# Optimization experiments

Measured on AMD Instinct MI355X. Metric: run time of the kernel, lower is better.

The kernel has to match this reference:

```python
import jax, jax.numpy as jnp
import numpy as np

EPS = 1e-08


def setup_inputs() -> dict:
    key = jax.random.key(0)
    k1, k2, k3 = jax.random.split(key, 3)
    B = 131072
    LIP_DIM = 20
    POSE_DIM = 6
    K = LIP_DIM + POSE_DIM  # 26
    return {
        "input": jax.random.normal(k1, (B, K), dtype=jnp.float32),
        "pose_weight": jax.random.normal(k2, (512, POSE_DIM), dtype=jnp.float32),
        "weight": jax.random.normal(k3, (512, LIP_DIM), dtype=jnp.float32),
    }


def reference(input, pose_weight, weight):
    # weight: (512, lip_dim), pose_weight: (512, pose_dim) -> (512, K)
    w = jnp.concatenate([weight, pose_weight], axis=-1) + EPS
    # reduced QR (torch.qr default): Q (512, K)
    Q, R = jnp.linalg.qr(w, mode="reduced")
    Q = Q.astype(jnp.float32)
    # Original: sum_k diag_embed(input) @ Q.T over dim=1
    #   == for each batch b: sum_k input[b,k] * Q[:,k] == input @ Q.T
    # Fused equivalent avoids the (B, K, K) / (B, K, 512) intermediates.
    out = input @ Q.T  # (B, 512)
    return out
```

## Files before the change

kernel.cpp:

```cpp
#include <hip/hip_runtime.h>
#include <hip/hip_bf16.h>

#define EPSV 1e-8f
#define WSTRIDE 516

typedef float f32x4 __attribute__((ext_vector_type(4)));

__device__ __forceinline__ float rdlane(float v, int l) {
    return __int_as_float(__builtin_amdgcn_readlane(__float_as_int(v), l));
}

__device__ __forceinline__ void load_w_row(const float* __restrict__ lip_w,
                                           const float* __restrict__ pose_w,
                                           int row, float* w) {
    const float4* lp4 = reinterpret_cast<const float4*>(lip_w + row * 20);
    float4 t0 = lp4[0], t1 = lp4[1], t2 = lp4[2], t3 = lp4[3], t4 = lp4[4];
    const float2* pp2 = reinterpret_cast<const float2*>(pose_w + row * 6);
    float2 u0 = pp2[0], u1 = pp2[1], u2 = pp2[2];
    w[0]  = t0.x + EPSV; w[1]  = t0.y + EPSV; w[2]  = t0.z + EPSV; w[3]  = t0.w + EPSV;
    w[4]  = t1.x + EPSV; w[5]  = t1.y + EPSV; w[6]  = t1.z + EPSV; w[7]  = t1.w + EPSV;
    w[8]  = t2.x + EPSV; w[9]  = t2.y + EPSV; w[10] = t2.z + EPSV; w[11] = t2.w + EPSV;
    w[12] = t3.x + EPSV; w[13] = t3.y + EPSV; w[14] = t3.z + EPSV; w[15] = t3.w + EPSV;
    w[16] = t4.x + EPSV; w[17] = t4.y + EPSV; w[18] = t4.z + EPSV; w[19] = t4.w + EPSV;
    w[20] = u0.x + EPSV; w[21] = u0.y + EPSV;
    w[22] = u1.x + EPSV; w[23] = u1.y + EPSV;
    w[24] = u2.x + EPSV; w[25] = u2.y + EPSV;
}

template<int J>
struct QRStep {
    static __device__ __forceinline__ void run(float (&P)[26], float (&R)[26],
                                               const float (&Gr)[26], const int tid) {
        float sig = rdlane(Gr[J], J);
        float dot = 0.f;
#pragma unroll
        for (int i = 0; i < 26; ++i) {
            if (i < J) {
                const float rij = rdlane(R[i], J);
                sig = fmaf(-rij, rij, sig);
                dot = fmaf(rij, R[i], dot);
            }
        }
        const float alpha  = rdlane(P[J], J);
        const float S      = Gr[J] - dot - alpha * P[J];
        const float normx  = sqrtf(sig);
        const float beta   = (alpha >= 0.f) ? -normx : normx;
        const float tau    = (beta - alpha) / beta;
        const float rdenom = 1.f / (alpha - beta);
        const float dc     = fmaf(S, rdenom, P[J]);
        R[J] = (tid == J) ? beta : fmaf(-tau, dc, P[J]);
        const float trd = tau * rdenom;
#pragma unroll
        for (int i = 0; i < 26; ++i) {
            if (i > J) {
                const float pij = rdlane(P[i], J);
                P[i] = fmaf(-(trd * pij), dc, P[i]);
            }
        }
    }
};

template<int J> struct QRSteps {
    static __device__ __forceinline__ void run(float (&P)[26], float (&R)[26],
                                               const float (&Gr)[26], int tid) {
        QRStep<J>::run(P, R, Gr, tid);
        QRSteps<J + 1>::run(P, R, Gr, tid);
    }
};
template<> struct QRSteps<26> {
    static __device__ __forceinline__ void run(float (&)[26], float (&)[26],
                                               const float (&)[26], int) {}
};

__global__ __launch_bounds__(512) void qr_kernel(const float* __restrict__ pose_w,
                                                 const float* __restrict__ lip_w,
                                                 float* __restrict__ qt) {
    __shared__ float Wc[26 * WSTRIDE];
    __shared__ float G[26 * 27 + 8];
    __shared__ float Rlds[26][27];
    __shared__ float Rinv[26][27];

    const int tid = threadIdx.x;

    {
        float w[26];
        load_w_row(lip_w, pose_w, tid, w);
#pragma unroll
        for (int c = 0; c < 26; ++c) Wc[c * WSTRIDE + tid] = w[c];
    }
    __syncthreads();

    if (tid < 45) {
        int tm = 0, rem = tid;
        while (rem >= 9 - tm) { rem -= 9 - tm; ++tm; }
        const int tn = tm + rem;
        const int ra = (tm * 3 > 23) ? 23 : tm * 3;
        const int ca = (tn * 3 > 23) ? 23 : tn * 3;
        const f32x4* A0 = reinterpret_cast<const f32x4*>(&Wc[(ra + 0) * WSTRIDE]);
        const f32x4* A1 = reinterpret_cast<const f32x4*>(&Wc[(ra + 1) * WSTRIDE]);
        const f32x4* A2 = reinterpret_cast<const f32x4*>(&Wc[(ra + 2) * WSTRIDE]);
        const f32x4* B0 = reinterpret_cast<const f32x4*>(&Wc[(ca + 0) * WSTRIDE]);
        const f32x4* B1 = reinterpret_cast<const f32x4*>(&Wc[(ca + 1) * WSTRIDE]);
        const f32x4* B2 = reinterpret_cast<const f32x4*>(&Wc[(ca + 2) * WSTRIDE]);
        float acc[3][3] = {{0.f, 0.f, 0.f}, {0.f, 0.f, 0.f}, {0.f, 0.f, 0.f}};
#pragma unroll 4
        for (int i = 0; i < 128; ++i) {
            const f32x4 av[3] = {A0[i], A1[i], A2[i]};
            const f32x4 bv[3] = {B0[i], B1[i], B2[i]};
#pragma unroll
            for (int r = 0; r < 3; ++r) {
#pragma unroll
                for (int c = 0; c < 3; ++c) {
                    acc[r][c] = fmaf(av[r].x, bv[c].x, acc[r][c]);
                    acc[r][c] = fmaf(av[r].y, bv[c].y, acc[r][c]);
                    acc[r][c] = fmaf(av[r].z, bv[c].z, acc[r][c]);
                    acc[r][c] = fmaf(av[r].w, bv[c].w, acc[r][c]);
                }
            }
        }
#pragma unroll
        for (int r = 0; r < 3; ++r) {
#pragma unroll
            for (int c = 0; c < 3; ++c) {
                G[(ra + r) * 27 + (ca + c)] = acc[r][c];
                G[(ca + c) * 27 + (ra + r)] = acc[r][c];
            }
        }
    }
    __syncthreads();

    if (tid < 64) {
        const int cc = (tid < 26) ? tid : 25;
        float P[26], R[26], Gr[26];
        {
            const f32x4* pc = reinterpret_cast<const f32x4*>(&Wc[cc * WSTRIDE]);
            const f32x4 q0 = pc[0], q1 = pc[1], q2 = pc[2], q3 = pc[3],
                        q4 = pc[4], q5 = pc[5], q6 = pc[6];
            P[0]=q0.x;  P[1]=q0.y;  P[2]=q0.z;  P[3]=q0.w;
            P[4]=q1.x;  P[5]=q1.y;  P[6]=q1.z;  P[7]=q1.w;
            P[8]=q2.x;  P[9]=q2.y;  P[10]=q2.z; P[11]=q2.w;
            P[12]=q3.x; P[13]=q3.y; P[14]=q3.z; P[15]=q3.w;
            P[16]=q4.x; P[17]=q4.y; P[18]=q4.z; P[19]=q4.w;
            P[20]=q5.x; P[21]=q5.y; P[22]=q5.z; P[23]=q5.w;
            P[24]=q6.x; P[25]=q6.y;
        }
#pragma unroll
        for (int j = 0; j < 26; ++j) Gr[j] = G[j * 27 + cc];

        QRSteps<0>::run(P, R, Gr, tid);

        if (tid < 26) {
#pragma unroll
            for (int i = 0; i < 26; ++i)
                if (i <= tid) Rlds[i][tid] = R[i];
        }

        if (tid < 26) {
            float ri[26];
#pragma unroll
            for (int k = 25; k >= 0; --k) {
                float s = (k == tid) ? 1.f : 0.f;
#pragma unroll
                for (int m = 25; m > k; --m)
                    if (m <= tid) s = fmaf(-Rlds[k][m], ri[m], s);
                ri[k] = s / Rlds[k][k];
            }
#pragma unroll
            for (int k = 0; k < 26; ++k)
                if (k <= tid) Rinv[k][tid] = ri[k];
        }
    }
    __syncthreads();

    if (tid < 128) {
        float w0[26], w1[26], w2[26], w3[26];
        load_w_row(lip_w, pose_w, tid,       w0);
        load_w_row(lip_w, pose_w, tid + 128, w1);
        load_w_row(lip_w, pose_w, tid + 256, w2);
        load_w_row(lip_w, pose_w, tid + 384, w3);
#pragma unroll
        for (int k = 0; k < 26; ++k) {
            float q0 = 0.f, q1 = 0.f, q2 = 0.f, q3 = 0.f;
#pragma unroll
            for (int m = 0; m < 26; ++m) {
                if (m <= k) {
                    const float r = Rinv[m][k];
                    q0 = fmaf(w0[m], r, q0);
                    q1 = fmaf(w1[m], r, q1);
                    q2 = fmaf(w2[m], r, q2);
                    q3 = fmaf(w3[m], r, q3);
                }
            }
            float* qk = qt + k * 512 + tid;
            qk[0]   = q0;
            qk[128] = q1;
            qk[256] = q2;
            qk[384] = q3;
        }
    }
}


__global__ __launch_bounds__(256) void out_gemm(const float* __restrict__ in,
                                                const float* __restrict__ qt,
                                                float* __restrict__ out) {
    __shared__ float xs[832];
    const int tid = threadIdx.x;
    const long base = (long)blockIdx.x * 32;

    const float4* ip4 = reinterpret_cast<const float4*>(in + base * 26);
    if (tid < 208) reinterpret_cast<float4*>(xs)[tid] = ip4[tid];

    const int cg = tid & 127;
    const int rh = tid >> 7;

    float4 qf[26];
#pragma unroll
    for (int k = 0; k < 26; ++k)
        qf[k] = *reinterpret_cast<const float4*>(qt + k * 512 + cg * 4);
    __syncthreads();

    float* op = out + (base + (long)rh * 16) * 512 + cg * 4;
#pragma unroll
    for (int r = 0; r < 16; ++r) {
        const float* xr = xs + (rh * 16 + r) * 26;
        float ax = 0.f, ay = 0.f, az = 0.f, aw = 0.f;
#pragma unroll
        for (int k = 0; k < 26; ++k) {
            const float x = xr[k];
            ax = fmaf(x, qf[k].x, ax);
            ay = fmaf(x, qf[k].y, ay);
            az = fmaf(x, qf[k].z, az);
            aw = fmaf(x, qf[k].w, aw);
        }
        f32x4 o;
        o.x = ax; o.y = ay; o.z = az; o.w = aw;
        __builtin_nontemporal_store(o, reinterpret_cast<f32x4*>(op + (long)r * 512));
    }
}


extern "C" void kernel_launch(void* const* d_in, const int* in_sizes, int n_in,
                              void* d_out, int out_size, void* d_ws, size_t ws_size,
                              hipStream_t stream) {
    const float* input  = (const float*)d_in[0];
    const float* pose_w = (const float*)d_in[1];
    const float* lip_w  = (const float*)d_in[2];
    float* out = (float*)d_out;
    float* qt  = (float*)d_ws;

    const int B = in_sizes[0] / 26;

    qr_kernel<<<1, 512, 0, stream>>>(pose_w, lip_w, qt);
    out_gemm<<<(B + 31) / 32, 256, 0, stream>>>(input, qt, out);
}
```

Before: 82.45 us.

## Split Gram reduction across all waves and vectorize LDS reads in output GEMM

```diff
diff --git a/kernel.cpp b/kernel.cpp
--- a/kernel.cpp
+++ b/kernel.cpp
@@ -76,11 +76,14 @@
                                                  const float* __restrict__ lip_w,
                                                  float* __restrict__ qt) {
     __shared__ float Wc[26 * WSTRIDE];
+    __shared__ float Gp[8][26][27];
     __shared__ float G[26 * 27 + 8];
     __shared__ float Rlds[26][27];
     __shared__ float Rinv[26][27];
 
-    const int tid = threadIdx.x;
+    const int tid  = threadIdx.x;
+    const int lane = tid & 63;
+    const int wid  = tid >> 6;
 
     {
         float w[26];
@@ -90,8 +93,8 @@
     }
     __syncthreads();
 
-    if (tid < 45) {
-        int tm = 0, rem = tid;
+    if (lane < 45) {
+        int tm = 0, rem = lane;
         while (rem >= 9 - tm) { rem -= 9 - tm; ++tm; }
         const int tn = tm + rem;
         const int ra = (tm * 3 > 23) ? 23 : tm * 3;
@@ -103,8 +106,10 @@
         const f32x4* B1 = reinterpret_cast<const f32x4*>(&Wc[(ca + 1) * WSTRIDE]);
         const f32x4* B2 = reinterpret_cast<const f32x4*>(&Wc[(ca + 2) * WSTRIDE]);
         float acc[3][3] = {{0.f, 0.f, 0.f}, {0.f, 0.f, 0.f}, {0.f, 0.f, 0.f}};
+        const int i0 = 16 * wid;
 #pragma unroll 4
-        for (int i = 0; i < 128; ++i) {
+        for (int ii = 0; ii < 16; ++ii) {
+            const int i = i0 + ii;
             const f32x4 av[3] = {A0[i], A1[i], A2[i]};
             const f32x4 bv[3] = {B0[i], B1[i], B2[i]};
 #pragma unroll
@@ -122,10 +127,22 @@
         for (int r = 0; r < 3; ++r) {
 #pragma unroll
             for (int c = 0; c < 3; ++c) {
-                G[(ra + r) * 27 + (ca + c)] = acc[r][c];
-                G[(ca + c) * 27 + (ra + r)] = acc[r][c];
-            }
-        }
+                Gp[wid][ra + r][ca + c] = acc[r][c];
+                Gp[wid][ca + c][ra + r] = acc[r][c];
+            }
+        }
+    }
+    __syncthreads();
+
+    if (tid < 351) {
+        int r = 0, t = tid;
+        while (t >= 26 - r) { t -= 26 - r; ++r; }
+        const int c = r + t;
+        float s = 0.f;
+#pragma unroll
+        for (int w8 = 0; w8 < 8; ++w8) s += Gp[w8][r][c];
+        G[r * 27 + c] = s;
+        G[c * 27 + r] = s;
     }
     __syncthreads();
 
@@ -204,38 +221,61 @@
 __global__ __launch_bounds__(256) void out_gemm(const float* __restrict__ in,
                                                 const float* __restrict__ qt,
                                                 float* __restrict__ out) {
-    __shared__ float xs[832];
+    __shared__ __align__(16) float xs[32 * 28];
     const int tid = threadIdx.x;
     const long base = (long)blockIdx.x * 32;
 
-    const float4* ip4 = reinterpret_cast<const float4*>(in + base * 26);
-    if (tid < 208) reinterpret_cast<float4*>(xs)[tid] = ip4[tid];
+    if (tid < 208) {
+        const float4 v = reinterpret_cast<const float4*>(in + base * 26)[tid];
+        const float vals[4] = {v.x, v.y, v.z, v.w};
+        const int e0 = tid * 4;
+#pragma unroll
+        for (int q = 0; q < 4; ++q) {
+            const int e = e0 + q;
+            const int r = e / 26;
+            const int c = e - r * 26;
+            xs[r * 28 + c] = vals[q];
+        }
+    }
 
     const int cg = tid & 127;
     const int rh = tid >> 7;
 
-    float4 qf[26];
+    f32x4 qf[26];
 #pragma unroll
     for (int k = 0; k < 26; ++k)
-        qf[k] = *reinterpret_cast<const float4*>(qt + k * 512 + cg * 4);
+        qf[k] = *reinterpret_cast<const f32x4*>(qt + k * 512 + cg * 4);
     __syncthreads();
 
     float* op = out + (base + (long)rh * 16) * 512 + cg * 4;
 #pragma unroll
     for (int r = 0; r < 16; ++r) {
-        const float* xr = xs + (rh * 16 + r) * 26;
-        float ax = 0.f, ay = 0.f, az = 0.f, aw = 0.f;
+        const float* xr = xs + (rh * 16 + r) * 28;
+        const f32x4 t0 = *reinterpret_cast<const f32x4*>(xr + 0);
+        const f32x4 t1 = *reinterpret_cast<const f32x4*>(xr + 4);
+        const f32x4 t2 = *reinterpret_cast<const f32x4*>(xr + 8);
+        const f32x4 t3 = *reinterpret_cast<const f32x4*>(xr + 12);
+        const f32x4 t4 = *reinterpret_cast<const f32x4*>(xr + 16);
+        const f32x4 t5 = *reinterpret_cast<const f32x4*>(xr + 20);
+        const f32x4 t6 = *reinterpret_cast<const f32x4*>(xr + 24);
+        float xv[26];
+        xv[0]=t0.x;  xv[1]=t0.y;  xv[2]=t0.z;  xv[3]=t0.w;
+        xv[4]=t1.x;  xv[5]=t1.y;  xv[6]=t1.z;  xv[7]=t1.w;
+        xv[8]=t2.x;  xv[9]=t2.y;  xv[10]=t2.z; xv[11]=t2.w;
+        xv[12]=t3.x; xv[13]=t3.y; xv[14]=t3.z; xv[15]=t3.w;
+        xv[16]=t4.x; xv[17]=t4.y; xv[18]=t4.z; xv[19]=t4.w;
+        xv[20]=t5.x; xv[21]=t5.y; xv[22]=t5.z; xv[23]=t5.w;
+        xv[24]=t6.x; xv[25]=t6.y;
+        f32x4 acc = {0.f, 0.f, 0.f, 0.f};
 #pragma unroll
         for (int k = 0; k < 26; ++k) {
-            const float x = xr[k];
-            ax = fmaf(x, qf[k].x, ax);
-            ay = fmaf(x, qf[k].y, ay);
-            az = fmaf(x, qf[k].z, az);
-            aw = fmaf(x, qf[k].w, aw);
-        }
-        f32x4 o;
-        o.x = ax; o.y = ay; o.z = az; o.w = aw;
-        __builtin_nontemporal_store(o, reinterpret_cast<f32x4*>(op + (long)r * 512));
+            acc.x = fmaf(xv[k], qf[k].x, acc.x);
+            acc.y = fmaf(xv[k], qf[k].y, acc.y);
+            acc.z = fmaf(xv[k], qf[k].z, acc.z);
+            acc.w = fmaf(xv[k], qf[k].w, acc.w);
+        }
+        __builtin_nontemporal_store(acc,
+            reinterpret_cast<f32x4*>(op + (long)r * 512));
     }
 }
 
```

Result: faster. 72.76 us (-11.8%).
